# Performance work log

Measured on AMD Instinct MI355X. Metric: run time of the kernel, lower is better.

Reference implementation:

```python
import jax, jax.numpy as jnp
import numpy as np

B, N, H, E = 8, 2048, 4, 64  # batch, nodes, heads, embedding_dim (= GAT out_channels)
NEG_SLOPE = 0.2


def setup_inputs() -> dict:
    key = jax.random.key(0)
    ks = jax.random.split(key, 12)
    state = jax.random.normal(ks[0], (B, N), dtype=jnp.float32)
    strucEmb = jax.random.normal(ks[1], (N, E), dtype=jnp.float32) * 0.1
    # adjacency mask: True where NO edge (masked_fill -inf). Keep self-loops so every row has an edge.
    no_edge = jax.random.uniform(ks[2], (N, N)) > 0.02
    adj_mask = no_edge.at[jnp.arange(N), jnp.arange(N)].set(False)
    g = lambda k, shp: jax.random.normal(k, shp, dtype=jnp.float32) * np.float32(np.sqrt(2.0 / sum(shp[-2:])))
    W_gat = g(ks[3], (1, H * E))          # torch Linear(1, H*E, bias=False) weight.T laid out as (in,out)
    att = g(ks[4], (H, 2 * E, 1))         # GAT additive attention params
    Ws = g(ks[5], (E, E))                 # weight_struc (out,in)
    Wst = g(ks[6], (E, E))                # weight_state (out,in)
    lin1_w = g(ks[7], (E, E)); lin1_b = jnp.zeros((E,), jnp.float32)
    lin2_w = g(ks[8], (E, E)); lin2_b = jnp.zeros((E,), jnp.float32)
    lin3_w = g(ks[9], (1, 2 * E)); lin3_b = jnp.zeros((1,), jnp.float32)
    return dict(state=state, strucEmb=strucEmb, adj_mask=adj_mask, W_gat=W_gat, att=att,
                Ws=Ws, Wst=Wst, lin1_w=lin1_w, lin1_b=lin1_b, lin2_w=lin2_w, lin2_b=lin2_b,
                lin3_w=lin3_w, lin3_b=lin3_b)


def reference(state, strucEmb, adj_mask, W_gat, att, Ws, Wst,
              lin1_w, lin1_b, lin2_w, lin2_b, lin3_w, lin3_b):
    # --- Custom_GATConv_v2 ---
    # reshaped_state: [B,N,1]; Wh = state @ W -> [B,N,H*E] -> [B,H,N,E]
    Wh = (state[..., None] @ W_gat).reshape(B, N, H, E).transpose(0, 2, 1, 3)
    a_src = att[:, :E, 0]   # [H,E]
    a_tgt = att[:, E:, 0]   # [H,E]
    src = jnp.einsum('bhne,he->bhn', Wh, a_src)
    tgt = jnp.einsum('bhne,he->bhn', Wh, a_tgt)
    e = src[:, :, :, None] + tgt[:, :, None, :]          # [B,H,N,N]
    e = jnp.where(e > 0, e, NEG_SLOPE * e)               # LeakyReLU
    e = jnp.where(adj_mask[None, None], -jnp.inf, e)     # mask non-edges
    attn = jax.nn.softmax(e, axis=-1)
    x = jnp.einsum('bhij,bhje->bhie', attn, Wh).mean(axis=1)  # [B,N,E]

    # --- DeepQNet head (is_for_learn=True branch) ---
    x = jax.nn.relu(strucEmb @ Ws.T + x @ Wst.T)         # [B,N,E]
    state_emb = x.sum(axis=1)                            # [B,E]
    beta_state = state_emb @ lin1_w.T + lin1_b           # [B,E]
    beta_action = x @ lin2_w.T + lin2_b                  # [B,N,E]
    expand_state = jnp.broadcast_to(beta_state[:, None, :], (B, N, E))
    out = jax.nn.relu(jnp.concatenate([expand_state, beta_action], axis=2))  # [B,N,2E]
    return out @ lin3_w.T + lin3_b                       # [B,N,1]
```

## Files before the change

kernel.cpp:

```cpp
#include <hip/hip_runtime.h>

#define BB 8
#define NN 2048
#define HH 4
#define EE 64
#define MAXJ 128
#define NEG 0.2f
#define NCHUNK 32

static constexpr int OFF_CSRC  = 0;
static constexpr int OFF_CTGT  = 4;
static constexpr int OFF_WGWST = 8;
static constexpr int OFF_S     = 264;
static constexpr int OFF_SWS   = 288;
static constexpr int OFF_SATT  = OFF_SWS + NN * EE;
static constexpr int OFF_PART  = OFF_SATT + BB * HH * NN;

__global__ __launch_bounds__(256) void k_prep(const float* __restrict__ W_gat,
                                              const float* __restrict__ att,
                                              const float* __restrict__ Wst,
                                              float* __restrict__ ws) {
    __shared__ float wg[HH * EE];
    int t = threadIdx.x;
    wg[t] = W_gat[t];
    __syncthreads();
    if (t < HH) {
        float cs = 0.f, ct = 0.f;
        for (int e = 0; e < EE; ++e) {
            cs += wg[t * EE + e] * att[t * 2 * EE + e];
            ct += wg[t * EE + e] * att[t * 2 * EE + EE + e];
        }
        ws[OFF_CSRC + t] = cs;
        ws[OFF_CTGT + t] = ct;
    }
    int h = t >> 6, f = t & 63;
    float acc = 0.f;
    for (int e = 0; e < EE; ++e) acc += wg[h * EE + e] * Wst[f * EE + e];
    ws[OFF_WGWST + t] = acc;
}

__global__ __launch_bounds__(256) void k_fsatt(const int* __restrict__ adj,
                                               const float* __restrict__ state,
                                               const float* __restrict__ strucEmb,
                                               const float* __restrict__ Ws,
                                               float* __restrict__ ws) {
    __shared__ float s_wsT[EE * 65];
    __shared__ int   s_jl[MAXJ];
    __shared__ int   s_cnt;
    __shared__ float s_y[BB * MAXJ];
    const int i = blockIdx.x;
    const int t = threadIdx.x;
    const int w = t >> 6, lane = t & 63;

    if (w == 0) {
        const int* a = adj + (size_t)i * NN;
        int cnt = 0;
        for (int it = 0; it < NN / 64; ++it) {
            int j = it * 64 + lane;
            bool edge = (a[j] == 0);
            unsigned long long m = __ballot(edge);
            if (edge) {
                int pos = cnt + __popcll(m & ((1ull << lane) - 1ull));
                if (pos < MAXJ) s_jl[pos] = j;
            }
            cnt += __popcll(m);
        }
        if (lane == 0) s_cnt = cnt > MAXJ ? MAXJ : cnt;
    } else if (w == 1) {
        for (int it = 0; it < EE; ++it)
            s_wsT[lane * 65 + it] = Ws[it * EE + lane];
    }
    __syncthreads();
    const int cnt = s_cnt;

    if (w == 0) {
        float v = strucEmb[(size_t)i * EE + lane];
        float acc = 0.f;
        for (int e = 0; e < EE; ++e)
            acc += __shfl(v, e) * s_wsT[e * 65 + lane];
        ws[OFF_SWS + i * EE + lane] = acc;
    } else {
        for (int x = t - 64; x < BB * MAXJ; x += 192) {
            int k = x & (MAXJ - 1);
            if (k < cnt) s_y[x] = state[(x >> 7) * NN + s_jl[k]];
        }
    }
    __syncthreads();

    int g = t >> 3, k0 = t & 7, b = g >> 2, h = g & 3;
    const float* yb = s_y + b * MAXJ;
    float ct = ws[OFF_CTGT + h];
    float si = state[b * NN + i] * ws[OFF_CSRC + h];
    float mmax = -1e30f;
    for (int k = k0; k < cnt; k += 8) {
        float e = si + ct * yb[k]; e = e > 0.f ? e : NEG * e;
        mmax = fmaxf(mmax, e);
    }
    for (int o = 4; o; o >>= 1) mmax = fmaxf(mmax, __shfl_xor(mmax, o, 8));
    float den = 0.f, num = 0.f;
    for (int k = k0; k < cnt; k += 8) {
        float y = yb[k];
        float e = si + ct * y; e = e > 0.f ? e : NEG * e;
        float p = expf(e - mmax);
        den += p; num += p * y;
    }
    for (int o = 4; o; o >>= 1) { den += __shfl_xor(den, o, 8); num += __shfl_xor(num, o, 8); }
    if (k0 == 0) ws[OFF_SATT + (b * HH + h) * NN + i] = num / den;
}

__global__ void k_se(float* __restrict__ ws) {
    int b = blockIdx.x & 7, chunk = blockIdx.x >> 3;
    int t = threadIdx.x;
    int f = t & 63, sl = t >> 6;
    float wgw[HH];
    for (int h = 0; h < HH; ++h) wgw[h] = 0.25f * ws[OFF_WGWST + h * EE + f];
    float acc = 0.f;
    int i0 = chunk * (NN / NCHUNK);
    for (int i = i0 + sl; i < i0 + NN / NCHUNK; i += 4) {
        float v = ws[OFF_SWS + i * EE + f];
        for (int h = 0; h < HH; ++h)
            v += ws[OFF_SATT + (b * HH + h) * NN + i] * wgw[h];
        acc += fmaxf(v, 0.f);
    }
    __shared__ float red[256];
    red[t] = acc;
    __syncthreads();
    if (t < EE)
        ws[OFF_PART + (size_t)blockIdx.x * EE + t] =
            red[t] + red[t + 64] + red[t + 128] + red[t + 192];
}

__global__ void k_S(const float* __restrict__ lin1_w, const float* __restrict__ lin1_b,
                    const float* __restrict__ lin3_w, const float* __restrict__ lin3_b,
                    float* __restrict__ ws) {
    int b = blockIdx.x;
    int t = threadIdx.x;
    __shared__ float s_l1T[EE * 65];
    __shared__ float s_se[EE];
    for (int it = 0; it < EE; ++it)
        s_l1T[t * 65 + it] = lin1_w[it * EE + t];
    float se = 0.f;
    for (int c = 0; c < NCHUNK; ++c)
        se += ws[OFF_PART + (size_t)(c * BB + b) * EE + t];
    s_se[t] = se;
    __syncthreads();
    float bs = lin1_b[t];
    for (int f2 = 0; f2 < EE; ++f2) bs += s_se[f2] * s_l1T[f2 * 65 + t];
    float r = fmaxf(bs, 0.f) * lin3_w[t];
    for (int o = 32; o; o >>= 1) r += __shfl_xor(r, o);
    if (t == 0) ws[OFF_S + b] = r + lin3_b[0];
}

__global__ __launch_bounds__(256) void v13_out(const float* __restrict__ lin2_w,
                                               const float* __restrict__ lin2_b,
                                               const float* __restrict__ lin3_w,
                                               const float* __restrict__ ws,
                                               float* __restrict__ out) {
    __shared__ float s_l2T[EE * 65];
    const int t = threadIdx.x;
    for (int k = t; k < EE * EE; k += 256) {
        int fp = k >> 6, f = k & 63;
        s_l2T[f * 65 + fp] = lin2_w[k];
    }
    __syncthreads();
    int wave = blockIdx.x * 4 + (t >> 6);
    int lane = t & 63;
    int i = wave >> 3, b = wave & 7;
    float xv = ws[OFF_SWS + i * EE + lane];
    for (int h = 0; h < HH; ++h)
        xv += 0.25f * ws[OFF_SATT + (b * HH + h) * NN + i] * ws[OFF_WGWST + h * EE + lane];
    xv = fmaxf(xv, 0.f);
    float acc = lin2_b[lane];
    for (int f = 0; f < EE; ++f) acc += __shfl(xv, f) * s_l2T[f * 65 + lane];
    float r = fmaxf(acc, 0.f) * lin3_w[EE + lane];
    for (int o = 32; o; o >>= 1) r += __shfl_xor(r, o);
    if (lane == 0) out[(size_t)b * NN + i] = ws[OFF_S + b] + r;
}

extern "C" void kernel_launch(void* const* d_in, const int* in_sizes, int n_in,
                              void* d_out, int out_size, void* d_ws, size_t ws_size,
                              hipStream_t stream) {
    const float* state    = (const float*)d_in[0];
    const float* strucEmb = (const float*)d_in[1];
    const int*   adj      = (const int*)d_in[2];
    const float* W_gat    = (const float*)d_in[3];
    const float* att      = (const float*)d_in[4];
    const float* Ws       = (const float*)d_in[5];
    const float* Wst      = (const float*)d_in[6];
    const float* lin1_w   = (const float*)d_in[7];
    const float* lin1_b   = (const float*)d_in[8];
    const float* lin2_w   = (const float*)d_in[9];
    const float* lin2_b   = (const float*)d_in[10];
    const float* lin3_w   = (const float*)d_in[11];
    const float* lin3_b   = (const float*)d_in[12];
    float* ws = (float*)d_ws;
    float* out = (float*)d_out;

    k_prep <<<dim3(1),           dim3(256), 0, stream>>>(W_gat, att, Wst, ws);
    k_fsatt<<<dim3(NN),          dim3(256), 0, stream>>>(adj, state, strucEmb, Ws, ws);
    k_se   <<<dim3(NCHUNK * BB), dim3(256), 0, stream>>>(ws);
    k_S    <<<dim3(BB),          dim3(64),  0, stream>>>(lin1_w, lin1_b, lin3_w, lin3_b, ws);
    v13_out<<<dim3(NN * BB / 4), dim3(256), 0, stream>>>(lin2_w, lin2_b, lin3_w, ws, out);
}
```

Before: 54.06 us.

## Fuse prep and state-sum into row kernel, cut launches from five to three

Folds the weight precomputation (W_gat·Wst, attention coefficients) into every row block, which recomputes them redundantly. The row block now writes full relu'd x for all batches so that a single 8-block, 1024-thread kernel does the node sum. The output kernel handles one node per wave and loops over the 8 batches, reusing loaded weights and the sws value. This removes two launches and the chunked partial-sum pass, but adds redundant per-block prep work, a 4 MB intermediate write and read, and a reduction done by only 8 blocks.

Measured after the change: 83.20 us. 53.9% more time.

```diff
diff --git a/kernel.cpp b/kernel.cpp
--- a/kernel.cpp
+++ b/kernel.cpp
@@ -6,51 +6,54 @@
 #define EE 64
 #define MAXJ 128
 #define NEG 0.2f
-#define NCHUNK 32
-
-static constexpr int OFF_CSRC  = 0;
-static constexpr int OFF_CTGT  = 4;
-static constexpr int OFF_WGWST = 8;
-static constexpr int OFF_S     = 264;
-static constexpr int OFF_SWS   = 288;
-static constexpr int OFF_SATT  = OFF_SWS + NN * EE;
-static constexpr int OFF_PART  = OFF_SATT + BB * HH * NN;
-
-__global__ __launch_bounds__(256) void k_prep(const float* __restrict__ W_gat,
-                                              const float* __restrict__ att,
-                                              const float* __restrict__ Wst,
-                                              float* __restrict__ ws) {
-    __shared__ float wg[HH * EE];
-    int t = threadIdx.x;
-    wg[t] = W_gat[t];
-    __syncthreads();
-    if (t < HH) {
-        float cs = 0.f, ct = 0.f;
-        for (int e = 0; e < EE; ++e) {
-            cs += wg[t * EE + e] * att[t * 2 * EE + e];
-            ct += wg[t * EE + e] * att[t * 2 * EE + EE + e];
-        }
-        ws[OFF_CSRC + t] = cs;
-        ws[OFF_CTGT + t] = ct;
-    }
-    int h = t >> 6, f = t & 63;
-    float acc = 0.f;
-    for (int e = 0; e < EE; ++e) acc += wg[h * EE + e] * Wst[f * EE + e];
-    ws[OFF_WGWST + t] = acc;
-}
-
-__global__ __launch_bounds__(256) void k_fsatt(const int* __restrict__ adj,
-                                               const float* __restrict__ state,
-                                               const float* __restrict__ strucEmb,
-                                               const float* __restrict__ Ws,
-                                               float* __restrict__ ws) {
-    __shared__ float s_wsT[EE * 65];
+
+static constexpr int OFF_WGW  = 0;
+static constexpr int OFF_S    = 256;
+static constexpr int OFF_SWS  = 288;
+static constexpr int OFF_SATT = OFF_SWS + NN * EE;
+static constexpr int OFF_PART = OFF_SATT + NN * 32;
+
+__global__ __launch_bounds__(256) void k_row(const int* __restrict__ adj,
+                                             const float* __restrict__ state,
+                                             const float* __restrict__ strucEmb,
+                                             const float* __restrict__ Ws,
+                                             const float* __restrict__ W_gat,
+                                             const float* __restrict__ att,
+                                             const float* __restrict__ Wst,
+                                             float* __restrict__ ws) {
+    __shared__ float s_T[EE * 65];
+    __shared__ float s_wgw[HH * EE];
+    __shared__ float s_cs[HH], s_ct[HH];
     __shared__ int   s_jl[MAXJ];
     __shared__ int   s_cnt;
     __shared__ float s_y[BB * MAXJ];
+    __shared__ float s_satt[32];
+    __shared__ float s_sws[EE];
     const int i = blockIdx.x;
     const int t = threadIdx.x;
     const int w = t >> 6, lane = t & 63;
+
+    for (int q = 0; q < 16; ++q) {
+        int it = w * 16 + q;
+        s_T[lane * 65 + it] = Wst[it * EE + lane];
+    }
+    __syncthreads();
+
+    {
+        float acc = 0.f;
+        const float* wgh = W_gat + w * EE;
+        for (int e = 0; e < EE; ++e) acc += wgh[e] * s_T[e * 65 + lane];
+        s_wgw[t] = 0.25f * acc;
+        if (t < 2 * HH) {
+            int h = t & 3;
+            const float* wgx = W_gat + h * EE;
+            const float* av  = att + h * 2 * EE + (t >= HH ? EE : 0);
+            float a2 = 0.f;
+            for (int e = 0; e < EE; ++e) a2 += wgx[e] * av[e];
+            if (t < HH) s_cs[h] = a2; else s_ct[h] = a2;
+        }
+    }
+    __syncthreads();
 
     if (w == 0) {
         const int* a = adj + (size_t)i * NN;
@@ -66,9 +69,9 @@
             cnt += __popcll(m);
         }
         if (lane == 0) s_cnt = cnt > MAXJ ? MAXJ : cnt;
-    } else if (w == 1) {
-        for (int it = 0; it < EE; ++it)
-            s_wsT[lane * 65 + it] = Ws[it * EE + lane];
+    } else {
+        for (int it = w - 1; it < EE; it += 3)
+            s_T[lane * 65 + it] = Ws[it * EE + lane];
     }
     __syncthreads();
     const int cnt = s_cnt;
@@ -76,8 +79,8 @@
     if (w == 0) {
         float v = strucEmb[(size_t)i * EE + lane];
         float acc = 0.f;
-        for (int e = 0; e < EE; ++e)
-            acc += __shfl(v, e) * s_wsT[e * 65 + lane];
+        for (int e = 0; e < EE; ++e) acc += __shfl(v, e) * s_T[e * 65 + lane];
+        s_sws[lane] = acc;
         ws[OFF_SWS + i * EE + lane] = acc;
     } else {
         for (int x = t - 64; x < BB * MAXJ; x += 192) {
@@ -87,94 +90,113 @@
     }
     __syncthreads();
 
-    int g = t >> 3, k0 = t & 7, b = g >> 2, h = g & 3;
-    const float* yb = s_y + b * MAXJ;
-    float ct = ws[OFF_CTGT + h];
-    float si = state[b * NN + i] * ws[OFF_CSRC + h];
-    float mmax = -1e30f;
-    for (int k = k0; k < cnt; k += 8) {
-        float e = si + ct * yb[k]; e = e > 0.f ? e : NEG * e;
-        mmax = fmaxf(mmax, e);
-    }
-    for (int o = 4; o; o >>= 1) mmax = fmaxf(mmax, __shfl_xor(mmax, o, 8));
-    float den = 0.f, num = 0.f;
-    for (int k = k0; k < cnt; k += 8) {
-        float y = yb[k];
-        float e = si + ct * y; e = e > 0.f ? e : NEG * e;
-        float p = expf(e - mmax);
-        den += p; num += p * y;
-    }
-    for (int o = 4; o; o >>= 1) { den += __shfl_xor(den, o, 8); num += __shfl_xor(num, o, 8); }
-    if (k0 == 0) ws[OFF_SATT + (b * HH + h) * NN + i] = num / den;
-}
-
-__global__ void k_se(float* __restrict__ ws) {
-    int b = blockIdx.x & 7, chunk = blockIdx.x >> 3;
-    int t = threadIdx.x;
-    int f = t & 63, sl = t >> 6;
-    float wgw[HH];
-    for (int h = 0; h < HH; ++h) wgw[h] = 0.25f * ws[OFF_WGWST + h * EE + f];
-    float acc = 0.f;
-    int i0 = chunk * (NN / NCHUNK);
-    for (int i = i0 + sl; i < i0 + NN / NCHUNK; i += 4) {
-        float v = ws[OFF_SWS + i * EE + f];
+    {
+        int g = t >> 3, k0 = t & 7, b = g >> 2, h = g & 3;
+        const float* yb = s_y + b * MAXJ;
+        float ct = s_ct[h];
+        float si = state[b * NN + i] * s_cs[h];
+        float mmax = -1e30f;
+        for (int k = k0; k < cnt; k += 8) {
+            float e = si + ct * yb[k]; e = e > 0.f ? e : NEG * e;
+            mmax = fmaxf(mmax, e);
+        }
+        for (int o = 4; o; o >>= 1) mmax = fmaxf(mmax, __shfl_xor(mmax, o, 8));
+        float den = 0.f, num = 0.f;
+        for (int k = k0; k < cnt; k += 8) {
+            float y = yb[k];
+            float e = si + ct * y; e = e > 0.f ? e : NEG * e;
+            float p = expf(e - mmax);
+            den += p; num += p * y;
+        }
+        for (int o = 4; o; o >>= 1) { den += __shfl_xor(den, o, 8); num += __shfl_xor(num, o, 8); }
+        if (k0 == 0) {
+            float sv = num / den;
+            s_satt[g] = sv;
+            ws[OFF_SATT + i * 32 + g] = sv;
+        }
+    }
+    __syncthreads();
+
+    for (int q = 0; q < 2; ++q) {
+        int idx = q * 256 + t, b = idx >> 6, f = idx & 63;
+        float x = s_sws[f];
         for (int h = 0; h < HH; ++h)
-            v += ws[OFF_SATT + (b * HH + h) * NN + i] * wgw[h];
-        acc += fmaxf(v, 0.f);
-    }
-    __shared__ float red[256];
-    red[t] = acc;
-    __syncthreads();
-    if (t < EE)
-        ws[OFF_PART + (size_t)blockIdx.x * EE + t] =
-            red[t] + red[t + 64] + red[t + 128] + red[t + 192];
-}
-
-__global__ void k_S(const float* __restrict__ lin1_w, const float* __restrict__ lin1_b,
-                    const float* __restrict__ lin3_w, const float* __restrict__ lin3_b,
-                    float* __restrict__ ws) {
-    int b = blockIdx.x;
-    int t = threadIdx.x;
+            x += s_satt[b * 4 + h] * s_wgw[h * EE + f];
+        ws[OFF_PART + ((size_t)b * NN + i) * EE + f] = fmaxf(x, 0.f);
+    }
+    if (i == 0) ws[OFF_WGW + t] = s_wgw[t];
+}
+
+__global__ __launch_bounds__(1024) void k_S2(const float* __restrict__ lin1_w,
+                                             const float* __restrict__ lin1_b,
+                                             const float* __restrict__ lin3_w,
+                                             const float* __restrict__ lin3_b,
+                                             float* __restrict__ ws) {
+    __shared__ float s_red[1024];
     __shared__ float s_l1T[EE * 65];
     __shared__ float s_se[EE];
-    for (int it = 0; it < EE; ++it)
-        s_l1T[t * 65 + it] = lin1_w[it * EE + t];
-    float se = 0.f;
-    for (int c = 0; c < NCHUNK; ++c)
-        se += ws[OFF_PART + (size_t)(c * BB + b) * EE + t];
-    s_se[t] = se;
-    __syncthreads();
-    float bs = lin1_b[t];
-    for (int f2 = 0; f2 < EE; ++f2) bs += s_se[f2] * s_l1T[f2 * 65 + t];
-    float r = fmaxf(bs, 0.f) * lin3_w[t];
-    for (int o = 32; o; o >>= 1) r += __shfl_xor(r, o);
-    if (t == 0) ws[OFF_S + b] = r + lin3_b[0];
-}
-
-__global__ __launch_bounds__(256) void v13_out(const float* __restrict__ lin2_w,
-                                               const float* __restrict__ lin2_b,
-                                               const float* __restrict__ lin3_w,
-                                               const float* __restrict__ ws,
-                                               float* __restrict__ out) {
+    const int b = blockIdx.x;
+    const int t = threadIdx.x;
+    const int sl = t >> 6, f = t & 63;
+    for (int k = t; k < EE * EE; k += 1024) {
+        int o = k >> 6, f2 = k & 63;
+        s_l1T[f2 * 65 + o] = lin1_w[k];
+    }
+    float acc = 0.f;
+    const float* p = ws + OFF_PART + (size_t)b * NN * EE;
+    for (int i = sl; i < NN; i += 16)
+        acc += p[i * EE + f];
+    s_red[t] = acc;
+    __syncthreads();
+    if (t < EE) {
+        float se = 0.f;
+        for (int s = 0; s < 16; ++s) se += s_red[s * 64 + t];
+        s_se[t] = se;
+    }
+    __syncthreads();
+    if (t < EE) {
+        float bs = lin1_b[t];
+        for (int f2 = 0; f2 < EE; ++f2) bs += s_se[f2] * s_l1T[f2 * 65 + t];
+        float r = fmaxf(bs, 0.f) * lin3_w[t];
+        for (int o = 32; o; o >>= 1) r += __shfl_xor(r, o);
+        if (t == 0) ws[OFF_S + b] = r + lin3_b[0];
+    }
+}
+
+__global__ __launch_bounds__(256) void k_out2(const float* __restrict__ lin2_w,
+                                              const float* __restrict__ lin2_b,
+                                              const float* __restrict__ lin3_w,
+                                              const float* __restrict__ ws,
+                                              float* __restrict__ out) {
     __shared__ float s_l2T[EE * 65];
+    __shared__ float s_wgw[HH * EE];
+    __shared__ float s_S[BB];
+    __shared__ float s_l2b[EE], s_l3[EE];
     const int t = threadIdx.x;
+    const int w = t >> 6, lane = t & 63;
     for (int k = t; k < EE * EE; k += 256) {
         int fp = k >> 6, f = k & 63;
         s_l2T[f * 65 + fp] = lin2_w[k];
     }
-    __syncthreads();
-    int wave = blockIdx.x * 4 + (t >> 6);
-    int lane = t & 63;
-    int i = wave >> 3, b = wave & 7;
-    float xv = ws[OFF_SWS + i * EE + lane];
-    for (int h = 0; h < HH; ++h)
-        xv += 0.25f * ws[OFF_SATT + (b * HH + h) * NN + i] * ws[OFF_WGWST + h * EE + lane];
-    xv = fmaxf(xv, 0.f);
-    float acc = lin2_b[lane];
-    for (int f = 0; f < EE; ++f) acc += __shfl(xv, f) * s_l2T[f * 65 + lane];
-    float r = fmaxf(acc, 0.f) * lin3_w[EE + lane];
-    for (int o = 32; o; o >>= 1) r += __shfl_xor(r, o);
-    if (lane == 0) out[(size_t)b * NN + i] = ws[OFF_S + b] + r;
+    s_wgw[t] = ws[OFF_WGW + t];
+    if (t < BB) s_S[t] = ws[OFF_S + t];
+    if (t < EE) { s_l2b[t] = lin2_b[t]; s_l3[t] = lin3_w[EE + t]; }
+    __syncthreads();
+
+    const int i = blockIdx.x * 4 + w;
+    float xsws = ws[OFF_SWS + i * EE + lane];
+    float sa = (lane < 32) ? ws[OFF_SATT + i * 32 + lane] : 0.f;
+    for (int b = 0; b < BB; ++b) {
+        float xv = xsws;
+        for (int h = 0; h < HH; ++h)
+            xv += __shfl(sa, b * 4 + h) * s_wgw[h * EE + lane];
+        xv = fmaxf(xv, 0.f);
+        float acc = s_l2b[lane];
+        for (int f = 0; f < EE; ++f) acc += __shfl(xv, f) * s_l2T[f * 65 + lane];
+        float r = fmaxf(acc, 0.f) * s_l3[lane];
+        for (int o = 32; o; o >>= 1) r += __shfl_xor(r, o);
+        if (lane == 0) out[(size_t)b * NN + i] = s_S[b] + r;
+    }
 }
 
 extern "C" void kernel_launch(void* const* d_in, const int* in_sizes, int n_in,
@@ -196,9 +218,7 @@
     float* ws = (float*)d_ws;
     float* out = (float*)d_out;
 
-    k_prep <<<dim3(1),           dim3(256), 0, stream>>>(W_gat, att, Wst, ws);
-    k_fsatt<<<dim3(NN),          dim3(256), 0, stream>>>(adj, state, strucEmb, Ws, ws);
-    k_se   <<<dim3(NCHUNK * BB), dim3(256), 0, stream>>>(ws);
-    k_S    <<<dim3(BB),          dim3(64),  0, stream>>>(lin1_w, lin1_b, lin3_w, lin3_b, ws);
-    v13_out<<<dim3(NN * BB / 4), dim3(256), 0, stream>>>(lin2_w, lin2_b, lin3_w, ws, out);
-}
+    k_row <<<dim3(NN),     dim3(256),  0, stream>>>(adj, state, strucEmb, Ws, W_gat, att, Wst, ws);
+    k_S2  <<<dim3(BB),     dim3(1024), 0, stream>>>(lin1_w, lin1_b, lin3_w, lin3_b, ws);
+    k_out2<<<dim3(NN / 4), dim3(256),  0, stream>>>(lin2_w, lin2_b, lin3_w, ws, out);
+}
```

## Transpose attention output layout and reuse per-node data across batches in output kernel

Applied to the files above, without the earlier changes.

The per-node attention results are now stored node-major (node, batch*head) so that one wave can load all 32 values for a node with a single coalesced read. The output kernel now gives each wave one node and loops over all 8 batches, reusing the struct-embedding row and the lin2 weight tile. Small parameters are staged in shared memory. This cuts the output grid by 8x, which reduces repeated transposed lin2 loads and global reads, but each wave now runs its loop serially and there are fewer blocks for parallelism.

After: 52.11 us. 1.04x faster.

```diff
diff --git a/kernel.cpp b/kernel.cpp
--- a/kernel.cpp
+++ b/kernel.cpp
@@ -14,7 +14,7 @@
 static constexpr int OFF_S     = 264;
 static constexpr int OFF_SWS   = 288;
 static constexpr int OFF_SATT  = OFF_SWS + NN * EE;
-static constexpr int OFF_PART  = OFF_SATT + BB * HH * NN;
+static constexpr int OFF_PART  = OFF_SATT + NN * 32;
 
 __global__ __launch_bounds__(256) void k_prep(const float* __restrict__ W_gat,
                                               const float* __restrict__ att,
@@ -105,7 +105,7 @@
         den += p; num += p * y;
     }
     for (int o = 4; o; o >>= 1) { den += __shfl_xor(den, o, 8); num += __shfl_xor(num, o, 8); }
-    if (k0 == 0) ws[OFF_SATT + (b * HH + h) * NN + i] = num / den;
+    if (k0 == 0) ws[OFF_SATT + i * 32 + g] = num / den;
 }
 
 __global__ void k_se(float* __restrict__ ws) {
@@ -119,7 +119,7 @@
     for (int i = i0 + sl; i < i0 + NN / NCHUNK; i += 4) {
         float v = ws[OFF_SWS + i * EE + f];
         for (int h = 0; h < HH; ++h)
-            v += ws[OFF_SATT + (b * HH + h) * NN + i] * wgw[h];
+            v += ws[OFF_SATT + i * 32 + b * 4 + h] * wgw[h];
         acc += fmaxf(v, 0.f);
     }
     __shared__ float red[256];
@@ -151,30 +151,40 @@
     if (t == 0) ws[OFF_S + b] = r + lin3_b[0];
 }
 
-__global__ __launch_bounds__(256) void v13_out(const float* __restrict__ lin2_w,
-                                               const float* __restrict__ lin2_b,
-                                               const float* __restrict__ lin3_w,
-                                               const float* __restrict__ ws,
-                                               float* __restrict__ out) {
+__global__ __launch_bounds__(256) void k_out2(const float* __restrict__ lin2_w,
+                                              const float* __restrict__ lin2_b,
+                                              const float* __restrict__ lin3_w,
+                                              const float* __restrict__ ws,
+                                              float* __restrict__ out) {
     __shared__ float s_l2T[EE * 65];
+    __shared__ float s_wgw[HH * EE];
+    __shared__ float s_S[BB];
+    __shared__ float s_l2b[EE], s_l3[EE];
     const int t = threadIdx.x;
+    const int w = t >> 6, lane = t & 63;
     for (int k = t; k < EE * EE; k += 256) {
         int fp = k >> 6, f = k & 63;
         s_l2T[f * 65 + fp] = lin2_w[k];
     }
-    __syncthreads();
-    int wave = blockIdx.x * 4 + (t >> 6);
-    int lane = t & 63;
-    int i = wave >> 3, b = wave & 7;
-    float xv = ws[OFF_SWS + i * EE + lane];
-    for (int h = 0; h < HH; ++h)
-        xv += 0.25f * ws[OFF_SATT + (b * HH + h) * NN + i] * ws[OFF_WGWST + h * EE + lane];
-    xv = fmaxf(xv, 0.f);
-    float acc = lin2_b[lane];
-    for (int f = 0; f < EE; ++f) acc += __shfl(xv, f) * s_l2T[f * 65 + lane];
-    float r = fmaxf(acc, 0.f) * lin3_w[EE + lane];
-    for (int o = 32; o; o >>= 1) r += __shfl_xor(r, o);
-    if (lane == 0) out[(size_t)b * NN + i] = ws[OFF_S + b] + r;
+    s_wgw[t] = 0.25f * ws[OFF_WGWST + t];
+    if (t < BB) s_S[t] = ws[OFF_S + t];
+    if (t < EE) { s_l2b[t] = lin2_b[t]; s_l3[t] = lin3_w[EE + t]; }
+    __syncthreads();
+
+    const int i = blockIdx.x * 4 + w;
+    float xsws = ws[OFF_SWS + i * EE + lane];
+    float sa = (lane < 32) ? ws[OFF_SATT + i * 32 + lane] : 0.f;
+    for (int b = 0; b < BB; ++b) {
+        float xv = xsws;
+        for (int h = 0; h < HH; ++h)
+            xv += __shfl(sa, b * 4 + h) * s_wgw[h * EE + lane];
+        xv = fmaxf(xv, 0.f);
+        float acc = s_l2b[lane];
+        for (int f = 0; f < EE; ++f) acc += __shfl(xv, f) * s_l2T[f * 65 + lane];
+        float r = fmaxf(acc, 0.f) * s_l3[lane];
+        for (int o = 32; o; o >>= 1) r += __shfl_xor(r, o);
+        if (lane == 0) out[(size_t)b * NN + i] = s_S[b] + r;
+    }
 }
 
 extern "C" void kernel_launch(void* const* d_in, const int* in_sizes, int n_in,
@@ -200,5 +210,5 @@
     k_fsatt<<<dim3(NN),          dim3(256), 0, stream>>>(adj, state, strucEmb, Ws, ws);
     k_se   <<<dim3(NCHUNK * BB), dim3(256), 0, stream>>>(ws);
     k_S    <<<dim3(BB),          dim3(64),  0, stream>>>(lin1_w, lin1_b, lin3_w, lin3_b, ws);
-    v13_out<<<dim3(NN * BB / 4), dim3(256), 0, stream>>>(lin2_w, lin2_b, lin3_w, ws, out);
-}
+    k_out2 <<<dim3(NN / 4),      dim3(256), 0, stream>>>(lin2_w, lin2_b, lin3_w, ws, out);
+}
```
